# Kernel optimization log

Hardware: AMD Instinct MI355X
Metric: run time of the kernel (lower is better)

The kernel has to match this reference:

```python
import jax, jax.numpy as jnp
import numpy as np

N, I, O, G = 16384, 128, 128, 16


def setup_inputs() -> dict:
    key = jax.random.key(0)
    k1, k2, k3 = jax.random.split(key, 3)
    coef_norm = np.sqrt(I) * np.sqrt(G)  # smooth_initialization=False
    return {
        "x": jax.random.normal(k1, (N, I), dtype=jnp.float32),
        "cos_amplitudes": jax.random.normal(k2, (O, I, G), dtype=jnp.float32) / coef_norm,
        "sin_amplitudes": jax.random.normal(k3, (O, I, G), dtype=jnp.float32) / coef_norm,
        "bias": jnp.zeros((O,), dtype=jnp.float32),
        "ln_gamma": jnp.ones((O,), dtype=jnp.float32),
        "ln_beta": jnp.zeros((O,), dtype=jnp.float32),
    }


def reference(x, cos_amplitudes, sin_amplitudes, bias, ln_gamma, ln_beta):
    g = cos_amplitudes.shape[-1]
    # frequencies buffer: init_freq_scale=1.0 -> [1, 2, ..., grid_size]
    freqs = jnp.arange(1, g + 1, dtype=x.dtype)  # (G,)
    phases = x[:, :, None] * freqs               # (N, I, G)
    # contraction expressed as a GEMM instead of broadcast-sum over (N,O,I,G)
    out = jnp.einsum("nig,oig->no", jnp.cos(phases), cos_amplitudes)
    out = out + jnp.einsum("nig,oig->no", jnp.sin(phases), sin_amplitudes)
    out = out + bias  # (N, O)
    # LayerNorm over output_dim, eps=1e-5 (torch default)
    mu = jnp.mean(out, axis=-1, keepdims=True)
    var = jnp.var(out, axis=-1, keepdims=True)
    out = (out - mu) / jnp.sqrt(var + 1e-5) * ln_gamma + ln_beta
    return out
```

## Files before the change

### kernel.cpp

```cpp
#include <hip/hip_runtime.h>
#include <hip/hip_bf16.h>
#include <math.h>

#define N_TOK 16384
#define I_DIM 128
#define O_DIM 128
#define G_DIM 16
#define BN 64
#define CI 4
#define KC (CI * G_DIM * 2)
#define NCHUNK (I_DIM / CI)
#define A_STRIDE 136
#define B_STRIDE 136
#define C_STRIDE 132

typedef __bf16 bf16x8 __attribute__((ext_vector_type(8)));
typedef float  f32x4  __attribute__((ext_vector_type(4)));

__global__ __launch_bounds__(256) void fkan_pack_b(
    const float* __restrict__ cosA, const float* __restrict__ sinA,
    __hip_bfloat16* __restrict__ Bp)
{
    int idx = blockIdx.x * 256 + threadIdx.x;
    int kk = idx & 127;
    int o  = (idx >> 7) & 127;
    int c  = idx >> 14;
    int il = kk >> 5;
    int r  = kk & 31;
    int g  = r >> 1;
    int s  = r & 1;
    int i  = c * CI + il;
    const float* src = s ? sinA : cosA;
    float v = src[(o * I_DIM + i) * G_DIM + g];
    Bp[idx] = __float2bfloat16(v);
}

__global__ __launch_bounds__(256) void fkan_main(
    const float* __restrict__ x,
    const __hip_bfloat16* __restrict__ Bp,
    const float* __restrict__ bias,
    const float* __restrict__ gamma,
    const float* __restrict__ beta,
    float* __restrict__ out)
{
    __shared__ __align__(16) __bf16 smem[64 * A_STRIDE + 128 * B_STRIDE];
    __bf16* As = smem;
    __bf16* Bs = smem + 64 * A_STRIDE;
    float*  Cs = (float*)(smem + 64 * A_STRIDE);

    const int t    = threadIdx.x;
    const int lane = t & 63;
    const int wave = t >> 6;
    const int row16 = lane & 15;
    const int quad  = lane >> 4;
    const int n0 = blockIdx.x * BN;

    const int fn  = t >> 2;
    const int fil = t & 3;

    f32x4 acc[4][2];
#pragma unroll
    for (int mt = 0; mt < 4; ++mt)
#pragma unroll
        for (int ot = 0; ot < 2; ++ot)
            acc[mt][ot] = (f32x4){0.f, 0.f, 0.f, 0.f};

    for (int c = 0; c < NCHUNK; ++c) {
        {
            float xv = x[(size_t)(n0 + fn) * I_DIM + (c * CI + fil)];
            float s1, c1;
            __sincosf(xv, &s1, &c1);
            __align__(16) __bf16 feat[32];
            feat[0] = (__bf16)c1;
            feat[1] = (__bf16)s1;
            float ck = c1, sk = s1;
#pragma unroll
            for (int g = 1; g < 16; ++g) {
                float cn = ck * c1 - sk * s1;
                float sn = sk * c1 + ck * s1;
                feat[2 * g]     = (__bf16)cn;
                feat[2 * g + 1] = (__bf16)sn;
                ck = cn; sk = sn;
            }
            bf16x8* dst = (bf16x8*)(As + fn * A_STRIDE + fil * 32);
            const bf16x8* srcv = (const bf16x8*)feat;
#pragma unroll
            for (int j = 0; j < 4; ++j) dst[j] = srcv[j];
        }
        {
            const uint4* src = (const uint4*)(Bp + (size_t)c * (O_DIM * KC));
#pragma unroll
            for (int it = 0; it < 8; ++it) {
                int idx = it * 256 + t;
                uint4 v = src[idx];
                int o    = idx >> 4;
                int kk16 = idx & 15;
                *(uint4*)(Bs + o * B_STRIDE + kk16 * 8) = v;
            }
        }
        __syncthreads();

#pragma unroll
        for (int ks = 0; ks < 4; ++ks) {
            bf16x8 a[4], b[2];
#pragma unroll
            for (int mt = 0; mt < 4; ++mt)
                a[mt] = *(const bf16x8*)(As + (mt * 16 + row16) * A_STRIDE + ks * 32 + quad * 8);
#pragma unroll
            for (int ot = 0; ot < 2; ++ot)
                b[ot] = *(const bf16x8*)(Bs + (wave * 32 + ot * 16 + row16) * B_STRIDE + ks * 32 + quad * 8);
#pragma unroll
            for (int mt = 0; mt < 4; ++mt)
#pragma unroll
                for (int ot = 0; ot < 2; ++ot)
                    acc[mt][ot] = __builtin_amdgcn_mfma_f32_16x16x32_bf16(
                        a[mt], b[ot], acc[mt][ot], 0, 0, 0);
        }
        __syncthreads();
    }

#pragma unroll
    for (int mt = 0; mt < 4; ++mt)
#pragma unroll
        for (int ot = 0; ot < 2; ++ot)
#pragma unroll
            for (int r = 0; r < 4; ++r)
                Cs[(mt * 16 + quad * 4 + r) * C_STRIDE + wave * 32 + ot * 16 + row16] =
                    acc[mt][ot][r];
    __syncthreads();

    {
        const int r  = t >> 2;
        const int qt = t & 3;
        const float* crow = Cs + r * C_STRIDE + qt * 32;
        float vals[32];
        float sum = 0.f, sumsq = 0.f;
#pragma unroll
        for (int j = 0; j < 32; ++j) {
            float v = crow[j] + bias[qt * 32 + j];
            vals[j] = v;
            sum += v;
            sumsq += v * v;
        }
        sum   += __shfl_xor(sum, 1);   sum   += __shfl_xor(sum, 2);
        sumsq += __shfl_xor(sumsq, 1); sumsq += __shfl_xor(sumsq, 2);
        float mu  = sum * (1.0f / O_DIM);
        float var = sumsq * (1.0f / O_DIM) - mu * mu;
        float rstd = rsqrtf(var + 1e-5f);

        float* orow = out + (size_t)(n0 + r) * O_DIM + qt * 32;
#pragma unroll
        for (int jj = 0; jj < 8; ++jj) {
            float4 o4;
            o4.x = (vals[4 * jj + 0] - mu) * rstd * gamma[qt * 32 + 4 * jj + 0] + beta[qt * 32 + 4 * jj + 0];
            o4.y = (vals[4 * jj + 1] - mu) * rstd * gamma[qt * 32 + 4 * jj + 1] + beta[qt * 32 + 4 * jj + 1];
            o4.z = (vals[4 * jj + 2] - mu) * rstd * gamma[qt * 32 + 4 * jj + 2] + beta[qt * 32 + 4 * jj + 2];
            o4.w = (vals[4 * jj + 3] - mu) * rstd * gamma[qt * 32 + 4 * jj + 3] + beta[qt * 32 + 4 * jj + 3];
            *(float4*)(orow + 4 * jj) = o4;
        }
    }
}

extern "C" void kernel_launch(void* const* d_in, const int* in_sizes, int n_in,
                              void* d_out, int out_size, void* d_ws, size_t ws_size,
                              hipStream_t stream) {
    const float* x     = (const float*)d_in[0];
    const float* cosA  = (const float*)d_in[1];
    const float* sinA  = (const float*)d_in[2];
    const float* bias  = (const float*)d_in[3];
    const float* gamma = (const float*)d_in[4];
    const float* beta  = (const float*)d_in[5];
    float* out = (float*)d_out;

    __hip_bfloat16* Bp = (__hip_bfloat16*)d_ws;

    fkan_pack_b<<<dim3((NCHUNK * O_DIM * KC) / 256), dim3(256), 0, stream>>>(cosA, sinA, Bp);
    fkan_main<<<dim3(N_TOK / BN), dim3(256), 0, stream>>>(x, Bp, bias, gamma, beta, out);
}
```

Measured before the change: 113.7 us.

## Double-buffer features, load B fragments directly to registers, vectorize packing

The main kernel now preloads each thread's x row into registers, double-buffers the sin/cos feature tile in LDS, and loads B weight fragments straight from global memory into registers instead of staging them through shared memory. Features for the next chunk are computed while the current chunk's MFMAs run, leaving one barrier per iteration instead of two. The input-channel-to-chunk mapping is strided (i&31), and the pack kernel now uses float4 reads and uint4 writes with fewer threads. The trade-offs are more register pressure and uncoalesced, L2-dependent B loads issued by each wave.

```diff
diff --git a/kernel.cpp b/kernel.cpp
--- a/kernel.cpp
+++ b/kernel.cpp
@@ -7,11 +7,9 @@
 #define O_DIM 128
 #define G_DIM 16
 #define BN 64
-#define CI 4
-#define KC (CI * G_DIM * 2)
-#define NCHUNK (I_DIM / CI)
+#define KC 128
+#define NCHUNK 32
 #define A_STRIDE 136
-#define B_STRIDE 136
 #define C_STRIDE 132
 
 typedef __bf16 bf16x8 __attribute__((ext_vector_type(8)));
@@ -21,18 +19,22 @@
     const float* __restrict__ cosA, const float* __restrict__ sinA,
     __hip_bfloat16* __restrict__ Bp)
 {
-    int idx = blockIdx.x * 256 + threadIdx.x;
-    int kk = idx & 127;
-    int o  = (idx >> 7) & 127;
-    int c  = idx >> 14;
-    int il = kk >> 5;
-    int r  = kk & 31;
-    int g  = r >> 1;
-    int s  = r & 1;
-    int i  = c * CI + il;
-    const float* src = s ? sinA : cosA;
-    float v = src[(o * I_DIM + i) * G_DIM + g];
-    Bp[idx] = __float2bfloat16(v);
+    int u  = blockIdx.x * 256 + threadIdx.x;
+    int gq = u & 3;
+    int i  = (u >> 2) & 127;
+    int o  = u >> 9;
+    int base = (o * I_DIM + i) * G_DIM + gq * 4;
+    float4 cv = *(const float4*)(cosA + base);
+    float4 sv = *(const float4*)(sinA + base);
+    union { __bf16 h[8]; uint4 v; } w;
+    w.h[0] = (__bf16)cv.x; w.h[1] = (__bf16)sv.x;
+    w.h[2] = (__bf16)cv.y; w.h[3] = (__bf16)sv.y;
+    w.h[4] = (__bf16)cv.z; w.h[5] = (__bf16)sv.z;
+    w.h[6] = (__bf16)cv.w; w.h[7] = (__bf16)sv.w;
+    int c  = i & 31;
+    int il = i >> 5;
+    int kk0 = il * 32 + gq * 8;
+    *(uint4*)((__bf16*)Bp + (size_t)c * (O_DIM * KC) + o * KC + kk0) = w.v;
 }
 
 __global__ __launch_bounds__(256) void fkan_main(
@@ -43,20 +45,26 @@
     const float* __restrict__ beta,
     float* __restrict__ out)
 {
-    __shared__ __align__(16) __bf16 smem[64 * A_STRIDE + 128 * B_STRIDE];
-    __bf16* As = smem;
-    __bf16* Bs = smem + 64 * A_STRIDE;
-    float*  Cs = (float*)(smem + 64 * A_STRIDE);
+    __shared__ __align__(16) char smem[2 * 64 * A_STRIDE * 2];
+    __bf16* As = (__bf16*)smem;
+    float*  Cs = (float*)smem;
 
-    const int t    = threadIdx.x;
-    const int lane = t & 63;
-    const int wave = t >> 6;
+    const int t     = threadIdx.x;
+    const int lane  = t & 63;
+    const int wave  = t >> 6;
     const int row16 = lane & 15;
     const int quad  = lane >> 4;
-    const int n0 = blockIdx.x * BN;
+    const int n0    = blockIdx.x * BN;
 
     const int fn  = t >> 2;
     const int fil = t & 3;
+
+    float4 xr[8];
+    {
+        const float* xrow = x + (size_t)(n0 + fn) * I_DIM + fil * 32;
+#pragma unroll
+        for (int j = 0; j < 8; ++j) xr[j] = *(const float4*)(xrow + 4 * j);
+    }
 
     f32x4 acc[4][2];
 #pragma unroll
@@ -65,56 +73,62 @@
         for (int ot = 0; ot < 2; ++ot)
             acc[mt][ot] = (f32x4){0.f, 0.f, 0.f, 0.f};
 
+    auto stage_feats = [&](int c, int buf) {
+        const float* xf = (const float*)xr;
+        float xv = xf[c];
+        float s1, c1;
+        __sincosf(xv, &s1, &c1);
+        __align__(16) __bf16 feat[32];
+        feat[0] = (__bf16)c1;
+        feat[1] = (__bf16)s1;
+        float ck = c1, sk = s1;
+#pragma unroll
+        for (int g = 1; g < 16; ++g) {
+            float cn = ck * c1 - sk * s1;
+            float sn = sk * c1 + ck * s1;
+            feat[2 * g]     = (__bf16)cn;
+            feat[2 * g + 1] = (__bf16)sn;
+            ck = cn; sk = sn;
+        }
+        bf16x8* dst = (bf16x8*)(As + (size_t)buf * (64 * A_STRIDE) + fn * A_STRIDE + fil * 32);
+        const bf16x8* srcv = (const bf16x8*)feat;
+#pragma unroll
+        for (int j = 0; j < 4; ++j) dst[j] = srcv[j];
+    };
+
+    stage_feats(0, 0);
+    __syncthreads();
+
+    const __hip_bfloat16* Bw = Bp + (size_t)wave * 32 * KC;
+
     for (int c = 0; c < NCHUNK; ++c) {
+        const int buf = c & 1;
+
+        bf16x8 bfrag[4][2];
         {
-            float xv = x[(size_t)(n0 + fn) * I_DIM + (c * CI + fil)];
-            float s1, c1;
-            __sincosf(xv, &s1, &c1);
-            __align__(16) __bf16 feat[32];
-            feat[0] = (__bf16)c1;
-            feat[1] = (__bf16)s1;
-            float ck = c1, sk = s1;
+            const __bf16* Bq = (const __bf16*)(Bw + (size_t)c * (O_DIM * KC));
 #pragma unroll
-            for (int g = 1; g < 16; ++g) {
-                float cn = ck * c1 - sk * s1;
-                float sn = sk * c1 + ck * s1;
-                feat[2 * g]     = (__bf16)cn;
-                feat[2 * g + 1] = (__bf16)sn;
-                ck = cn; sk = sn;
-            }
-            bf16x8* dst = (bf16x8*)(As + fn * A_STRIDE + fil * 32);
-            const bf16x8* srcv = (const bf16x8*)feat;
+            for (int ks = 0; ks < 4; ++ks)
 #pragma unroll
-            for (int j = 0; j < 4; ++j) dst[j] = srcv[j];
+                for (int ot = 0; ot < 2; ++ot)
+                    bfrag[ks][ot] = *(const bf16x8*)(Bq + (ot * 16 + row16) * KC + ks * 32 + quad * 8);
         }
-        {
-            const uint4* src = (const uint4*)(Bp + (size_t)c * (O_DIM * KC));
-#pragma unroll
-            for (int it = 0; it < 8; ++it) {
-                int idx = it * 256 + t;
-                uint4 v = src[idx];
-                int o    = idx >> 4;
-                int kk16 = idx & 15;
-                *(uint4*)(Bs + o * B_STRIDE + kk16 * 8) = v;
-            }
-        }
-        __syncthreads();
 
+        if (c + 1 < NCHUNK) stage_feats(c + 1, buf ^ 1);
+
+        const __bf16* Ab = As + (size_t)buf * (64 * A_STRIDE);
 #pragma unroll
         for (int ks = 0; ks < 4; ++ks) {
-            bf16x8 a[4], b[2];
+            bf16x8 a[4];
 #pragma unroll
             for (int mt = 0; mt < 4; ++mt)
-                a[mt] = *(const bf16x8*)(As + (mt * 16 + row16) * A_STRIDE + ks * 32 + quad * 8);
-#pragma unroll
-            for (int ot = 0; ot < 2; ++ot)
-                b[ot] = *(const bf16x8*)(Bs + (wave * 32 + ot * 16 + row16) * B_STRIDE + ks * 32 + quad * 8);
+                a[mt] = *(const bf16x8*)(Ab + (mt * 16 + row16) * A_STRIDE + ks * 32 + quad * 8);
 #pragma unroll
             for (int mt = 0; mt < 4; ++mt)
 #pragma unroll
                 for (int ot = 0; ot < 2; ++ot)
                     acc[mt][ot] = __builtin_amdgcn_mfma_f32_16x16x32_bf16(
-                        a[mt], b[ot], acc[mt][ot], 0, 0, 0);
+                        a[mt], bfrag[ks][ot], acc[mt][ot], 0, 0, 0);
         }
         __syncthreads();
     }
@@ -174,6 +188,6 @@
 
     __hip_bfloat16* Bp = (__hip_bfloat16*)d_ws;
 
-    fkan_pack_b<<<dim3((NCHUNK * O_DIM * KC) / 256), dim3(256), 0, stream>>>(cosA, sinA, Bp);
+    fkan_pack_b<<<dim3((O_DIM * I_DIM * 4) / 256), dim3(256), 0, stream>>>(cosA, sinA, Bp);
     fkan_main<<<dim3(N_TOK / BN), dim3(256), 0, stream>>>(x, Bp, bias, gamma, beta, out);
 }
```

New measurement: 123.3 us. 8.5% more time.
